# Optimization experiments

Hardware: AMD Instinct MI355X
Metric: run time of the kernel (lower is better)

The kernel has to match this reference:

```python
import jax, jax.numpy as jnp
import numpy as np

B, H, D, N = 4, 16, 64, 2048

def setup_inputs() -> dict:
    key = jax.random.key(0)
    kq, kk, kv = jax.random.split(key, 3)
    q = jax.random.normal(kq, (B, H, D, N), dtype=jnp.float32)
    k = jax.random.normal(kk, (B, H, D, N), dtype=jnp.float32)
    v = jax.random.normal(kv, (B, H, D, N), dtype=jnp.float32)
    return {"q": q, "k": k, "v": v}

def reference(q, k, v):
    # layout: (b, h, d, n); scale uses head_dim = q.shape[-2]
    scale = q.shape[-2] ** (-0.5)
    sim = jnp.einsum('bhdi,bhdj->bhij', q * scale, k)  # [B,H,N,N]
    attn = jax.nn.softmax(sim, axis=-1)  # stable softmax (internally subtracts max)
    out = jnp.einsum('bhij,bhdj->bhdi', attn, v)  # [B,H,D,N]
    return out
```

## Files before the change

### kernel.cpp

```cpp
#include <hip/hip_runtime.h>


#define DDIM 64
#define NSEQ 2048
#define STR  72
#define ROWB (STR * 2)
#define BUFB (128 * ROWB)

typedef _Float16 half8   __attribute__((ext_vector_type(8)));
typedef _Float16 half4v  __attribute__((ext_vector_type(4)));
typedef _Float16 half2v  __attribute__((ext_vector_type(2)));
typedef float    float4v __attribute__((ext_vector_type(4)));

__global__ __launch_bounds__(512, 4) void attn_fwd(
    const float* __restrict__ qg, const float* __restrict__ kg,
    const float* __restrict__ vg, float* __restrict__ og) {
  __shared__ __align__(16) char smem[2 * BUFB];

  const int t    = threadIdx.x;
  const int lane = t & 63;
  const int w    = t >> 6;
  const int n16  = lane & 15;
  const int quad = lane >> 4;

  const int bid  = blockIdx.x;
  const int head = ((bid & 7) << 3) | (bid >> 6);
  const int tile = (bid >> 3) & 7;
  const int i0   = tile * 256;

  const float* qh = qg + (size_t)head * DDIM * NSEQ;
  const float* kh = kg + (size_t)head * DDIM * NSEQ;
  const float* vh = vg + (size_t)head * DDIM * NSEQ;

  const int dp = t & 31;
  const int iq = t >> 5;
  const int vd = t >> 3;
  const int vj = (t & 7) * 8;

  {
    _Float16* Qt = (_Float16*)smem;
    const float mul = 0.125f * 1.44269504088896340736f;
#pragma unroll
    for (int h = 0; h < 4; ++h) {
      const float* r0 = qh + (2 * dp) * NSEQ + i0 + h * 64 + iq * 4;
      float4v a = *(const float4v*)(r0);
      float4v b = *(const float4v*)(r0 + NSEQ);
      _Float16* base = Qt + (h * 64 + iq * 4) * STR + 2 * dp;
#pragma unroll
      for (int s = 0; s < 4; ++s) {
        half2v hh = {(_Float16)(a[s] * mul), (_Float16)(b[s] * mul)};
        *(half2v*)(base + s * STR) = hh;
      }
    }
  }
  __syncthreads();

  const _Float16* Qt = (const _Float16*)smem;
  const half8 bq00 = *(const half8*)(Qt + (w * 32 + n16) * STR + quad * 8);
  const half8 bq01 = *(const half8*)(Qt + (w * 32 + n16) * STR + 32 + quad * 8);
  const half8 bq10 = *(const half8*)(Qt + (w * 32 + 16 + n16) * STR + quad * 8);
  const half8 bq11 = *(const half8*)(Qt + (w * 32 + 16 + n16) * STR + 32 + quad * 8);
  __syncthreads();

  const half8 ones = {1.0f16, 1.0f16, 1.0f16, 1.0f16,
                      1.0f16, 1.0f16, 1.0f16, 1.0f16};

  float4v o0[4], o1[4];
  float4v lac0, lac1;
#pragma unroll
  for (int dt = 0; dt < 4; ++dt) {
    o0[dt] = (float4v){0.f, 0.f, 0.f, 0.f};
    o1[dt] = (float4v){0.f, 0.f, 0.f, 0.f};
  }
  lac0 = (float4v){0.f, 0.f, 0.f, 0.f};
  lac1 = (float4v){0.f, 0.f, 0.f, 0.f};

  const float* kp = kh + (2 * dp) * NSEQ + iq * 4;
  const float* vp = vh + vd * NSEQ + vj;
  float4v ka, kb, vr0, vr1;
  ka  = *(const float4v*)(kp);
  kb  = *(const float4v*)(kp + NSEQ);
  vr0 = *(const float4v*)(vp);
  vr1 = *(const float4v*)(vp + 4);

  {
    _Float16* Ktw = (_Float16*)(smem + BUFB);
    _Float16* base = Ktw + (iq * 4) * STR + 2 * dp;
#pragma unroll
    for (int s = 0; s < 4; ++s) {
      half2v hh = {(_Float16)ka[s], (_Float16)kb[s]};
      *(half2v*)(base + s * STR) = hh;
    }
    half8 hv = {(_Float16)vr0[0], (_Float16)vr0[1], (_Float16)vr0[2], (_Float16)vr0[3],
                (_Float16)vr1[0], (_Float16)vr1[1], (_Float16)vr1[2], (_Float16)vr1[3]};
    *(half8*)(Ktw + 64 * STR + vd * STR + vj) = hv;
  }
  __syncthreads();

  for (int kt = 0; kt < 32; ++kt) {
    const _Float16* Kt = (const _Float16*)(smem + ((kt + 1) & 1) * BUFB);
    const _Float16* Vt = Kt + 64 * STR;

    if (kt < 31) {
      const int j1 = (kt + 1) * 64;
      ka  = *(const float4v*)(kp + j1);
      kb  = *(const float4v*)(kp + NSEQ + j1);
      vr0 = *(const float4v*)(vp + j1);
      vr1 = *(const float4v*)(vp + j1 + 4);
    }

    half4v p0[4], p1[4];
#pragma unroll
    for (int jt = 0; jt < 4; ++jt) {
      half8 kfa = *(const half8*)(Kt + (jt * 16 + n16) * STR + quad * 8);
      half8 kfb = *(const half8*)(Kt + (jt * 16 + n16) * STR + 32 + quad * 8);
      float4v sa = {0.f, 0.f, 0.f, 0.f};
      sa = __builtin_amdgcn_mfma_f32_16x16x32_f16(kfa, bq00, sa, 0, 0, 0);
      sa = __builtin_amdgcn_mfma_f32_16x16x32_f16(kfb, bq01, sa, 0, 0, 0);
      float4v sb = {0.f, 0.f, 0.f, 0.f};
      sb = __builtin_amdgcn_mfma_f32_16x16x32_f16(kfa, bq10, sb, 0, 0, 0);
      sb = __builtin_amdgcn_mfma_f32_16x16x32_f16(kfb, bq11, sb, 0, 0, 0);
      p0[jt] = (half4v){(_Float16)__builtin_amdgcn_exp2f(sa[0]),
                        (_Float16)__builtin_amdgcn_exp2f(sa[1]),
                        (_Float16)__builtin_amdgcn_exp2f(sa[2]),
                        (_Float16)__builtin_amdgcn_exp2f(sa[3])};
      p1[jt] = (half4v){(_Float16)__builtin_amdgcn_exp2f(sb[0]),
                        (_Float16)__builtin_amdgcn_exp2f(sb[1]),
                        (_Float16)__builtin_amdgcn_exp2f(sb[2]),
                        (_Float16)__builtin_amdgcn_exp2f(sb[3])};
    }

    half8 pb0g0 = __builtin_shufflevector(p0[0], p0[1], 0, 1, 2, 3, 4, 5, 6, 7);
    half8 pb0g1 = __builtin_shufflevector(p0[2], p0[3], 0, 1, 2, 3, 4, 5, 6, 7);
    half8 pb1g0 = __builtin_shufflevector(p1[0], p1[1], 0, 1, 2, 3, 4, 5, 6, 7);
    half8 pb1g1 = __builtin_shufflevector(p1[2], p1[3], 0, 1, 2, 3, 4, 5, 6, 7);

    lac0 = __builtin_amdgcn_mfma_f32_16x16x32_f16(ones, pb0g0, lac0, 0, 0, 0);
    lac0 = __builtin_amdgcn_mfma_f32_16x16x32_f16(ones, pb0g1, lac0, 0, 0, 0);
    lac1 = __builtin_amdgcn_mfma_f32_16x16x32_f16(ones, pb1g0, lac1, 0, 0, 0);
    lac1 = __builtin_amdgcn_mfma_f32_16x16x32_f16(ones, pb1g1, lac1, 0, 0, 0);

#pragma unroll
    for (int dt = 0; dt < 4; ++dt) {
#pragma unroll
      for (int g = 0; g < 2; ++g) {
        half4v va0 = *(const half4v*)(Vt + (dt * 16 + n16) * STR + g * 32 + quad * 4);
        half4v va1 = *(const half4v*)(Vt + (dt * 16 + n16) * STR + g * 32 + 16 + quad * 4);
        half8 va = __builtin_shufflevector(va0, va1, 0, 1, 2, 3, 4, 5, 6, 7);
        o0[dt] = __builtin_amdgcn_mfma_f32_16x16x32_f16(
            va, g ? pb0g1 : pb0g0, o0[dt], 0, 0, 0);
        o1[dt] = __builtin_amdgcn_mfma_f32_16x16x32_f16(
            va, g ? pb1g1 : pb1g0, o1[dt], 0, 0, 0);
      }
    }

    if (kt < 31) {
      _Float16* Ktw = (_Float16*)(smem + (kt & 1) * BUFB);
      _Float16* base = Ktw + (iq * 4) * STR + 2 * dp;
#pragma unroll
      for (int s = 0; s < 4; ++s) {
        half2v hh = {(_Float16)ka[s], (_Float16)kb[s]};
        *(half2v*)(base + s * STR) = hh;
      }
      half8 hv = {(_Float16)vr0[0], (_Float16)vr0[1], (_Float16)vr0[2], (_Float16)vr0[3],
                  (_Float16)vr1[0], (_Float16)vr1[1], (_Float16)vr1[2], (_Float16)vr1[3]};
      *(half8*)(Ktw + 64 * STR + vd * STR + vj) = hv;
      __syncthreads();
    }
  }

  const float inv0 = 1.0f / lac0[0];
  const float inv1 = 1.0f / lac1[0];
  {
    float* ob = og + (size_t)head * DDIM * NSEQ + i0 + w * 32 + n16;
#pragma unroll
    for (int dt = 0; dt < 4; ++dt) {
#pragma unroll
      for (int r = 0; r < 4; ++r) {
        const size_t drow = (size_t)(dt * 16 + quad * 4 + r) * NSEQ;
        ob[drow]      = o0[dt][r] * inv0;
        ob[drow + 16] = o1[dt][r] * inv1;
      }
    }
  }
}

extern "C" void kernel_launch(void* const* d_in, const int* in_sizes, int n_in,
                              void* d_out, int out_size, void* d_ws, size_t ws_size,
                              hipStream_t stream) {
  (void)in_sizes; (void)n_in; (void)d_ws; (void)ws_size; (void)out_size;
  const float* q = (const float*)d_in[0];
  const float* k = (const float*)d_in[1];
  const float* v = (const float*)d_in[2];
  attn_fwd<<<dim3(512), dim3(512), 0, stream>>>(q, k, v, (float*)d_out);
}
```

Measured before the change: 210.0 us.

## Double threads per block: one 16-query tile per wave, split K/V loading

The block grows from 512 to 1024 threads, so each wave handles 16 query rows instead of 32, which halves per-thread accumulators and MFMA work. The first 512 threads prefetch and convert the K tile while the other 512 handle the V tile, so each thread does half the global loads per iteration. This trades register pressure and per-wave work for more waves to hide latency. It adds barrier cost across 16 waves and redundant K/V fragment LDS reads, since each K fragment now feeds only one query subtile.

Result: slower. 231.3 us (+10.2%).

```diff
diff --git a/kernel.cpp b/kernel.cpp
--- a/kernel.cpp
+++ b/kernel.cpp
@@ -12,7 +12,7 @@
 typedef _Float16 half2v  __attribute__((ext_vector_type(2)));
 typedef float    float4v __attribute__((ext_vector_type(4)));
 
-__global__ __launch_bounds__(512, 4) void attn_fwd(
+__global__ __launch_bounds__(1024, 8) void attn_fwd(
     const float* __restrict__ qg, const float* __restrict__ kg,
     const float* __restrict__ vg, float* __restrict__ og) {
   __shared__ __align__(16) char smem[2 * BUFB];
@@ -32,20 +32,30 @@
   const float* kh = kg + (size_t)head * DDIM * NSEQ;
   const float* vh = vg + (size_t)head * DDIM * NSEQ;
 
-  const int dp = t & 31;
-  const int iq = t >> 5;
-  const int vd = t >> 3;
-  const int vj = (t & 7) * 8;
+  const int  u   = t & 511;
+  const int  dp  = u & 31;
+  const int  iq  = u >> 5;
+  const int  vd  = u >> 3;
+  const int  vj  = (u & 7) * 8;
+  const bool isK = (t < 512);
+
+  const float* kp = kh + (2 * dp) * NSEQ + iq * 4;
+  const float* vp = vh + vd * NSEQ + vj;
+
+  float4v ra, rb;
+  if (isK) { ra = *(const float4v*)(kp);  rb = *(const float4v*)(kp + NSEQ); }
+  else     { ra = *(const float4v*)(vp);  rb = *(const float4v*)(vp + 4);    }
 
   {
     _Float16* Qt = (_Float16*)smem;
     const float mul = 0.125f * 1.44269504088896340736f;
+    const int iq2 = t >> 5;
 #pragma unroll
-    for (int h = 0; h < 4; ++h) {
-      const float* r0 = qh + (2 * dp) * NSEQ + i0 + h * 64 + iq * 4;
+    for (int h = 0; h < 2; ++h) {
+      const float* r0 = qh + (2 * dp) * NSEQ + i0 + h * 128 + iq2 * 4;
       float4v a = *(const float4v*)(r0);
       float4v b = *(const float4v*)(r0 + NSEQ);
-      _Float16* base = Qt + (h * 64 + iq * 4) * STR + 2 * dp;
+      _Float16* base = Qt + (h * 128 + iq2 * 4) * STR + 2 * dp;
 #pragma unroll
       for (int s = 0; s < 4; ++s) {
         half2v hh = {(_Float16)(a[s] * mul), (_Float16)(b[s] * mul)};
@@ -56,44 +66,33 @@
   __syncthreads();
 
   const _Float16* Qt = (const _Float16*)smem;
-  const half8 bq00 = *(const half8*)(Qt + (w * 32 + n16) * STR + quad * 8);
-  const half8 bq01 = *(const half8*)(Qt + (w * 32 + n16) * STR + 32 + quad * 8);
-  const half8 bq10 = *(const half8*)(Qt + (w * 32 + 16 + n16) * STR + quad * 8);
-  const half8 bq11 = *(const half8*)(Qt + (w * 32 + 16 + n16) * STR + 32 + quad * 8);
+  const half8 bq0 = *(const half8*)(Qt + (w * 16 + n16) * STR + quad * 8);
+  const half8 bq1 = *(const half8*)(Qt + (w * 16 + n16) * STR + 32 + quad * 8);
   __syncthreads();
 
   const half8 ones = {1.0f16, 1.0f16, 1.0f16, 1.0f16,
                       1.0f16, 1.0f16, 1.0f16, 1.0f16};
 
-  float4v o0[4], o1[4];
-  float4v lac0, lac1;
+  float4v o[4];
+  float4v lac;
 #pragma unroll
-  for (int dt = 0; dt < 4; ++dt) {
-    o0[dt] = (float4v){0.f, 0.f, 0.f, 0.f};
-    o1[dt] = (float4v){0.f, 0.f, 0.f, 0.f};
-  }
-  lac0 = (float4v){0.f, 0.f, 0.f, 0.f};
-  lac1 = (float4v){0.f, 0.f, 0.f, 0.f};
-
-  const float* kp = kh + (2 * dp) * NSEQ + iq * 4;
-  const float* vp = vh + vd * NSEQ + vj;
-  float4v ka, kb, vr0, vr1;
-  ka  = *(const float4v*)(kp);
-  kb  = *(const float4v*)(kp + NSEQ);
-  vr0 = *(const float4v*)(vp);
-  vr1 = *(const float4v*)(vp + 4);
+  for (int dt = 0; dt < 4; ++dt) o[dt] = (float4v){0.f, 0.f, 0.f, 0.f};
+  lac = (float4v){0.f, 0.f, 0.f, 0.f};
 
   {
     _Float16* Ktw = (_Float16*)(smem + BUFB);
-    _Float16* base = Ktw + (iq * 4) * STR + 2 * dp;
+    if (isK) {
+      _Float16* base = Ktw + (iq * 4) * STR + 2 * dp;
 #pragma unroll
-    for (int s = 0; s < 4; ++s) {
-      half2v hh = {(_Float16)ka[s], (_Float16)kb[s]};
-      *(half2v*)(base + s * STR) = hh;
+      for (int s = 0; s < 4; ++s) {
+        half2v hh = {(_Float16)ra[s], (_Float16)rb[s]};
+        *(half2v*)(base + s * STR) = hh;
+      }
+    } else {
+      half8 hv = {(_Float16)ra[0], (_Float16)ra[1], (_Float16)ra[2], (_Float16)ra[3],
+                  (_Float16)rb[0], (_Float16)rb[1], (_Float16)rb[2], (_Float16)rb[3]};
+      *(half8*)(Ktw + 64 * STR + vd * STR + vj) = hv;
     }
-    half8 hv = {(_Float16)vr0[0], (_Float16)vr0[1], (_Float16)vr0[2], (_Float16)vr0[3],
-                (_Float16)vr1[0], (_Float16)vr1[1], (_Float16)vr1[2], (_Float16)vr1[3]};
-    *(half8*)(Ktw + 64 * STR + vd * STR + vj) = hv;
   }
   __syncthreads();
 
@@ -103,42 +102,29 @@
 
     if (kt < 31) {
       const int j1 = (kt + 1) * 64;
-      ka  = *(const float4v*)(kp + j1);
-      kb  = *(const float4v*)(kp + NSEQ + j1);
-      vr0 = *(const float4v*)(vp + j1);
-      vr1 = *(const float4v*)(vp + j1 + 4);
+      if (isK) { ra = *(const float4v*)(kp + j1); rb = *(const float4v*)(kp + NSEQ + j1); }
+      else     { ra = *(const float4v*)(vp + j1); rb = *(const float4v*)(vp + j1 + 4);    }
     }
 
-    half4v p0[4], p1[4];
+    half4v p[4];
 #pragma unroll
     for (int jt = 0; jt < 4; ++jt) {
       half8 kfa = *(const half8*)(Kt + (jt * 16 + n16) * STR + quad * 8);
       half8 kfb = *(const half8*)(Kt + (jt * 16 + n16) * STR + 32 + quad * 8);
       float4v sa = {0.f, 0.f, 0.f, 0.f};
-      sa = __builtin_amdgcn_mfma_f32_16x16x32_f16(kfa, bq00, sa, 0, 0, 0);
-      sa = __builtin_amdgcn_mfma_f32_16x16x32_f16(kfb, bq01, sa, 0, 0, 0);
-      float4v sb = {0.f, 0.f, 0.f, 0.f};
-      sb = __builtin_amdgcn_mfma_f32_16x16x32_f16(kfa, bq10, sb, 0, 0, 0);
-      sb = __builtin_amdgcn_mfma_f32_16x16x32_f16(kfb, bq11, sb, 0, 0, 0);
-      p0[jt] = (half4v){(_Float16)__builtin_amdgcn_exp2f(sa[0]),
-                        (_Float16)__builtin_amdgcn_exp2f(sa[1]),
-                        (_Float16)__builtin_amdgcn_exp2f(sa[2]),
-                        (_Float16)__builtin_amdgcn_exp2f(sa[3])};
-      p1[jt] = (half4v){(_Float16)__builtin_amdgcn_exp2f(sb[0]),
-                        (_Float16)__builtin_amdgcn_exp2f(sb[1]),
-                        (_Float16)__builtin_amdgcn_exp2f(sb[2]),
-                        (_Float16)__builtin_amdgcn_exp2f(sb[3])};
+      sa = __builtin_amdgcn_mfma_f32_16x16x32_f16(kfa, bq0, sa, 0, 0, 0);
+      sa = __builtin_amdgcn_mfma_f32_16x16x32_f16(kfb, bq1, sa, 0, 0, 0);
+      p[jt] = (half4v){(_Float16)__builtin_amdgcn_exp2f(sa[0]),
+                       (_Float16)__builtin_amdgcn_exp2f(sa[1]),
+                       (_Float16)__builtin_amdgcn_exp2f(sa[2]),
+                       (_Float16)__builtin_amdgcn_exp2f(sa[3])};
     }
 
-    half8 pb0g0 = __builtin_shufflevector(p0[0], p0[1], 0, 1, 2, 3, 4, 5, 6, 7);
-    half8 pb0g1 = __builtin_shufflevector(p0[2], p0[3], 0, 1, 2, 3, 4, 5, 6, 7);
-    half8 pb1g0 = __builtin_shufflevector(p1[0], p1[1], 0, 1, 2, 3, 4, 5, 6, 7);
-    half8 pb1g1 = __builtin_shufflevector(p1[2], p1[3], 0, 1, 2, 3, 4, 5, 6, 7);
+    half8 pg0 = __builtin_shufflevector(p[0], p[1], 0, 1, 2, 3, 4, 5, 6, 7);
+    half8 pg1 = __builtin_shufflevector(p[2], p[3], 0, 1, 2, 3, 4, 5, 6, 7);
 
-    lac0 = __builtin_amdgcn_mfma_f32_16x16x32_f16(ones, pb0g0, lac0, 0, 0, 0);
-    lac0 = __builtin_amdgcn_mfma_f32_16x16x32_f16(ones, pb0g1, lac0, 0, 0, 0);
-    lac1 = __builtin_amdgcn_mfma_f32_16x16x32_f16(ones, pb1g0, lac1, 0, 0, 0);
-    lac1 = __builtin_amdgcn_mfma_f32_16x16x32_f16(ones, pb1g1, lac1, 0, 0, 0);
+    lac = __builtin_amdgcn_mfma_f32_16x16x32_f16(ones, pg0, lac, 0, 0, 0);
+    lac = __builtin_amdgcn_mfma_f32_16x16x32_f16(ones, pg1, lac, 0, 0, 0);
 
 #pragma unroll
     for (int dt = 0; dt < 4; ++dt) {
@@ -147,39 +133,37 @@
         half4v va0 = *(const half4v*)(Vt + (dt * 16 + n16) * STR + g * 32 + quad * 4);
         half4v va1 = *(const half4v*)(Vt + (dt * 16 + n16) * STR + g * 32 + 16 + quad * 4);
         half8 va = __builtin_shufflevector(va0, va1, 0, 1, 2, 3, 4, 5, 6, 7);
-        o0[dt] = __builtin_amdgcn_mfma_f32_16x16x32_f16(
-            va, g ? pb0g1 : pb0g0, o0[dt], 0, 0, 0);
-        o1[dt] = __builtin_amdgcn_mfma_f32_16x16x32_f16(
-            va, g ? pb1g1 : pb1g0, o1[dt], 0, 0, 0);
+        o[dt] = __builtin_amdgcn_mfma_f32_16x16x32_f16(
+            va, g ? pg1 : pg0, o[dt], 0, 0, 0);
       }
     }
 
     if (kt < 31) {
       _Float16* Ktw = (_Float16*)(smem + (kt & 1) * BUFB);
-      _Float16* base = Ktw + (iq * 4) * STR + 2 * dp;
+      if (isK) {
+        _Float16* base = Ktw + (iq * 4) * STR + 2 * dp;
 #pragma unroll
-      for (int s = 0; s < 4; ++s) {
-        half2v hh = {(_Float16)ka[s], (_Float16)kb[s]};
-        *(half2v*)(base + s * STR) = hh;
+        for (int s = 0; s < 4; ++s) {
+          half2v hh = {(_Float16)ra[s], (_Float16)rb[s]};
+          *(half2v*)(base + s * STR) = hh;
+        }
+      } else {
+        half8 hv = {(_Float16)ra[0], (_Float16)ra[1], (_Float16)ra[2], (_Float16)ra[3],
+                    (_Float16)rb[0], (_Float16)rb[1], (_Float16)rb[2], (_Float16)rb[3]};
+        *(half8*)(Ktw + 64 * STR + vd * STR + vj) = hv;
       }
-      half8 hv = {(_Float16)vr0[0], (_Float16)vr0[1], (_Float16)vr0[2], (_Float16)vr0[3],
-                  (_Float16)vr1[0], (_Float16)vr1[1], (_Float16)vr1[2], (_Float16)vr1[3]};
-      *(half8*)(Ktw + 64 * STR + vd * STR + vj) = hv;
       __syncthreads();
     }
   }
 
-  const float inv0 = 1.0f / lac0[0];
-  const float inv1 = 1.0f / lac1[0];
+  const float inv = 1.0f / lac[0];
   {
-    float* ob = og + (size_t)head * DDIM * NSEQ + i0 + w * 32 + n16;
+    float* ob = og + (size_t)head * DDIM * NSEQ + i0 + w * 16 + n16;
 #pragma unroll
     for (int dt = 0; dt < 4; ++dt) {
 #pragma unroll
       for (int r = 0; r < 4; ++r) {
-        const size_t drow = (size_t)(dt * 16 + quad * 4 + r) * NSEQ;
-        ob[drow]      = o0[dt][r] * inv0;
-        ob[drow + 16] = o1[dt][r] * inv1;
+        ob[(size_t)(dt * 16 + quad * 4 + r) * NSEQ] = o[dt][r] * inv;
       }
     }
   }
@@ -192,5 +176,5 @@
   const float* q = (const float*)d_in[0];
   const float* k = (const float*)d_in[1];
   const float* v = (const float*)d_in[2];
-  attn_fwd<<<dim3(512), dim3(512), 0, stream>>>(q, k, v, (float*)d_out);
+  attn_fwd<<<dim3(512), dim3(1024), 0, stream>>>(q, k, v, (float*)d_out);
 }
```
